# Kernel optimization log

Hardware: AMD Instinct MI355X
Metric: run time of the kernel (lower is better)

Reference implementation:

```python
import jax, jax.numpy as jnp
import numpy as np

# ---- config (matches init_kwargs) ----
L_LEVELS = 10          # int(log(8192/16)/log(2)) + 1
LEVEL_DIM = 4
BASE_RES = 16
LOG2_T = 21
BOUND = 2.0            # contract() output bound
DENSITY_BIAS = -1.0
RGB_PADDING = 0.001
DEG_VIEW = 4
PRIME1 = np.uint32(2654435761)
PRIME2 = np.uint32(805459861)


def _grid_meta():
    # torch-ngp GridEncoder layout: per-level scale = base*2^l - 1 (per_level_scale=2),
    # resolution = base*2^l, params = min(2^21, (res+1)^3) rounded up to multiple of 8.
    offsets, scales, res_list, sizes = [0], [], [], []
    for l in range(L_LEVELS):
        res = BASE_RES * (2 ** l)
        scales.append(float(res - 1))
        n = min(2 ** LOG2_T, (res + 1) ** 3)
        n = int(np.ceil(n / 8) * 8)
        res_list.append(res)
        sizes.append(n)
        offsets.append(offsets[-1] + n)
    return scales, res_list, sizes, offsets

GRID_SCALES, GRID_RES, GRID_SIZES, GRID_OFFSETS = _grid_meta()
TOTAL_PARAMS = GRID_OFFSETS[-1]  # 14995560
CORNERS = np.array([[(c >> d) & 1 for d in range(3)] for c in range(8)], dtype=np.int32)


def contract(x):
    # mipnerf360 contraction, output in [-2, 2]
    eps = jnp.finfo(x.dtype).eps
    x_mag_sq = jnp.maximum(eps, jnp.sum(x * x, axis=-1, keepdims=True))
    return jnp.where(x_mag_sq <= 1.0, x, ((2.0 * jnp.sqrt(x_mag_sq) - 1.0) / x_mag_sq) * x)


def pos_enc(x):
    # coord.pos_enc with identity, min_deg=0, max_deg=DEG_VIEW -> dim 3 + 3*2*4 = 27
    scales = 2.0 ** jnp.arange(DEG_VIEW, dtype=x.dtype)
    xb = (x[..., None, :] * scales[:, None]).reshape(x.shape[:-1] + (3 * DEG_VIEW,))
    four = jnp.sin(jnp.concatenate([xb, xb + 0.5 * jnp.pi], axis=-1))
    return jnp.concatenate([x, four], axis=-1)


def grid_encode(x01, embeddings):
    # x01: [N,3] in [0,1]; embeddings: [TOTAL_PARAMS, LEVEL_DIM]
    feats = []
    for l in range(L_LEVELS):
        pos = x01 * GRID_SCALES[l] + 0.5  # align_corners=False
        pos_floor = jnp.floor(pos)
        frac = pos - pos_floor            # trilinear weights, differentiable in x01
        pg = pos_floor.astype(jnp.int32)  # [N,3]
        res1 = GRID_RES[l] + 1
        size = GRID_SIZES[l]
        use_hash = (res1 ** 3) > size
        lvl_emb = embeddings[GRID_OFFSETS[l]:GRID_OFFSETS[l] + size]
        acc = jnp.zeros(x01.shape[:-1] + (LEVEL_DIM,), x01.dtype)
        for c in range(8):
            off = CORNERS[c]
            corner = pg + off[None, :]
            if use_hash:
                cu = corner.astype(jnp.uint32)
                idx = (cu[:, 0] ^ (cu[:, 1] * PRIME1) ^ (cu[:, 2] * PRIME2)) % jnp.uint32(size)
                idx = idx.astype(jnp.int32)
            else:
                idx = corner[:, 0] + corner[:, 1] * res1 + corner[:, 2] * (res1 * res1)
            w = jnp.prod(jnp.where(off[None, :] == 1, frac, 1.0 - frac), axis=-1)  # [N]
            acc = acc + w[:, None] * lvl_emb[idx]
        feats.append(acc)
    return jnp.concatenate(feats, axis=-1)  # [N, 40]


def setup_inputs() -> dict:
    key = jax.random.key(0)
    ks = jax.random.split(key, 10)
    R, S = 2048, 32
    coords = jax.random.normal(ks[0], (R, S, 3), jnp.float32) * 1.5
    viewdirs = jax.random.normal(ks[1], (R, 3), jnp.float32)
    viewdirs = viewdirs / jnp.linalg.norm(viewdirs, axis=-1, keepdims=True)
    embeddings = (jax.random.uniform(ks[2], (TOTAL_PARAMS, LEVEL_DIM), jnp.float32) * 2.0 - 1.0) * 1e-4

    def lin(k, fan_in, fan_out):
        k1, k2 = jax.random.split(k)
        lim = 1.0 / np.sqrt(fan_in)
        w = jax.random.uniform(k1, (fan_in, fan_out), jnp.float32, -lim, lim)
        b = jax.random.uniform(k2, (fan_out,), jnp.float32, -lim, lim)
        return w, b

    w_d1, b_d1 = lin(ks[3], L_LEVELS * LEVEL_DIM, 64)
    w_d2, b_d2 = lin(ks[4], 64, 256)
    DIR_DIM = 3 + 3 * 2 * DEG_VIEW  # 27
    w_r0, b_r0 = lin(ks[5], 256 + DIR_DIM, 256)          # 283 -> 256
    w_r1, b_r1 = lin(ks[6], 256 + 256 + DIR_DIM, 256)    # skip concat: 539 -> 256
    w_rgb, b_rgb = lin(ks[7], 256, 3)
    return dict(coords=coords, viewdirs=viewdirs, embeddings=embeddings,
                w_d1=w_d1, b_d1=b_d1, w_d2=w_d2, b_d2=b_d2,
                w_r0=w_r0, b_r0=b_r0, w_r1=w_r1, b_r1=b_r1,
                w_rgb=w_rgb, b_rgb=b_rgb)


def reference(coords, viewdirs, embeddings, w_d1, b_d1, w_d2, b_d2,
              w_r0, b_r0, w_r1, b_r1, w_rgb, b_rgb):
    shape = coords.shape[:-1]  # (rays, samples)
    cw = contract(coords) / BOUND          # coords_warped, in [-1, 1]
    x01 = (cw.reshape(-1, 3) + BOUND) / (2.0 * BOUND)  # encoder normalization with bound=2
    feats = grid_encode(x01, embeddings)               # [N, 40]
    h = jax.nn.relu(feats @ w_d1 + b_d1)
    x = h @ w_d2 + b_d2                                # [N, 256]
    raw_density = x[:, 0].reshape(shape)
    density = jax.nn.softplus(raw_density + DENSITY_BIAS)
    bottleneck = x.reshape(shape + (256,))
    dir_enc = pos_enc(viewdirs)                        # [rays, 27]
    dir_enc = jnp.broadcast_to(dir_enc[..., None, :], shape + (dir_enc.shape[-1],))
    inp = jnp.concatenate([bottleneck, dir_enc], axis=-1)  # [rays, S, 283]
    y = jax.nn.relu(inp @ w_r0 + b_r0)
    y = jnp.concatenate([y, inp], axis=-1)             # skip at layer i == skip_layer_dir == 0
    y = jax.nn.relu(y @ w_r1 + b_r1)
    rgb = jax.nn.sigmoid(y @ w_rgb + b_rgb)            # rgb_premultiplier=1, rgb_bias=0
    rgb = rgb * (1.0 + 2.0 * RGB_PADDING) - RGB_PADDING
    return cw, density, rgb
```

## Files before the change

kernel.cpp:

```cpp
#include <hip/hip_runtime.h>
#include <math.h>

#define NS 65536
#define NRAYS 2048

typedef __attribute__((ext_vector_type(8))) short short8;
typedef __attribute__((ext_vector_type(4))) float f32x4;
typedef unsigned short u16;

#define OFF_FEATS 0ull
#define OFF_HBF   10485760ull
#define OFF_DW0   85983232ull
#define OFF_DW1   88080384ull
#define OFF_WD2T  90177536ull
#define OFF_WR0T  90210304ull
#define OFF_WR1T  90341376ull

#define OUT_DENS 196608
#define OUT_RGB  262144

__device__ __forceinline__ u16 f2b(float f) {
    unsigned u = __builtin_bit_cast(unsigned, f);
    return (u16)((u + 0x7FFFu + ((u >> 16) & 1u)) >> 16);
}

__global__ __launch_bounds__(256) void cvt_weights(
    const float* __restrict__ w_d2, const float* __restrict__ w_r0,
    const float* __restrict__ w_r1, u16* __restrict__ wd2t,
    u16* __restrict__ wr0t, u16* __restrict__ wr1t)
{
    int idx = blockIdx.x * 256 + threadIdx.x;
    if (idx < 16384)  wd2t[idx] = f2b(w_d2[(idx & 63)  * 256 + (idx >> 6)]);
    if (idx < 65536)  wr0t[idx] = f2b(w_r0[(idx & 255) * 256 + (idx >> 8)]);
    if (idx < 131072) wr1t[idx] = f2b(w_r1[(idx & 511) * 256 + (idx >> 9)]);
}

__global__ __launch_bounds__(256) void dir_kernel(
    const float* __restrict__ viewdirs,
    const float* __restrict__ w_r0, const float* __restrict__ b_r0,
    const float* __restrict__ w_r1, const float* __restrict__ b_r1,
    float* __restrict__ dirW0, float* __restrict__ dirW1)
{
    __shared__ float de[27];
    int ray = blockIdx.x, t = threadIdx.x;
    if (t < 27) {
        float v;
        if (t < 3) v = viewdirs[3*ray + t];
        else {
            int k = (t - 3) % 12;
            float b = viewdirs[3*ray + (k % 3)] * (float)(1 << (k / 3));
            v = (t < 15) ? sinf(b) : sinf(b + 1.5707964f);
        }
        de[t] = v;
    }
    __syncthreads();
    float a0 = b_r0[t], a1 = b_r1[t];
#pragma unroll
    for (int d = 0; d < 27; ++d) {
        a0 = fmaf(de[d], w_r0[(256+d)*256 + t], a0);
        a1 = fmaf(de[d], w_r1[(512+d)*256 + t], a1);
    }
    dirW0[ray*256 + t] = a0;
    dirW1[ray*256 + t] = a1;
}

__global__ __launch_bounds__(256) void encode_kernel(
    const float* __restrict__ coords, const float* __restrict__ emb,
    float* __restrict__ cw_out, float* __restrict__ featsT)
{
    int t = threadIdx.x;
    int l = blockIdx.x >> 8;
    int i = ((blockIdx.x & 255) << 8) + t;
    float x = coords[3*i], y = coords[3*i+1], z = coords[3*i+2];
    float m2 = fmaxf(x*x + y*y + z*z, 1.1920928955078125e-07f);
    float cx = x, cy = y, cz = z;
    if (m2 > 1.0f) { float s = (2.0f*sqrtf(m2) - 1.0f)/m2; cx*=s; cy*=s; cz*=s; }
    cx *= 0.5f; cy *= 0.5f; cz *= 0.5f;
    if (l == 0) { cw_out[3*i]=cx; cw_out[3*i+1]=cy; cw_out[3*i+2]=cz; }
    float u0 = (cx + 2.0f)*0.25f, u1 = (cy + 2.0f)*0.25f, u2 = (cz + 2.0f)*0.25f;

    int res = 16 << l;
    int res1 = res + 1;
    float scale = (float)(res - 1);
    unsigned off = (l >= 3) ? 315496u + (unsigned)(l-3)*2097152u
                            : (l == 0 ? 0u : (l == 1 ? 4920u : 40864u));
    float p0 = u0*scale + 0.5f, p1 = u1*scale + 0.5f, p2 = u2*scale + 0.5f;
    float f0 = floorf(p0), f1 = floorf(p1), f2 = floorf(p2);
    float fr0 = p0-f0, fr1 = p1-f1, fr2 = p2-f2;
    unsigned g0 = (unsigned)(int)f0, g1 = (unsigned)(int)f1, g2 = (unsigned)(int)f2;
    float a0=0.f, a1=0.f, a2=0.f, a3=0.f;
    bool use_hash = (l >= 3);
#pragma unroll
    for (int c = 0; c < 8; ++c) {
        unsigned ox = c & 1u, oy = (c >> 1) & 1u, oz = (c >> 2) & 1u;
        unsigned qx = g0 + ox, qy = g1 + oy, qz = g2 + oz;
        unsigned idx;
        if (use_hash) idx = (qx ^ (qy*2654435761u) ^ (qz*805459861u)) & 2097151u;
        else          idx = qx + qy*(unsigned)res1 + qz*(unsigned)(res1*res1);
        const float4 e = *(const float4*)(emb + 4u*(off + idx));
        float w = (ox ? fr0 : 1.0f-fr0) * (oy ? fr1 : 1.0f-fr1) * (oz ? fr2 : 1.0f-fr2);
        a0 = fmaf(w, e.x, a0); a1 = fmaf(w, e.y, a1);
        a2 = fmaf(w, e.z, a2); a3 = fmaf(w, e.w, a3);
    }
    featsT[(4*l+0)*NS + i] = a0;
    featsT[(4*l+1)*NS + i] = a1;
    featsT[(4*l+2)*NS + i] = a2;
    featsT[(4*l+3)*NS + i] = a3;
}

__global__ __launch_bounds__(256) void gemm_d1_kernel(
    const float* __restrict__ featsT, const float* __restrict__ w_d1,
    const float* __restrict__ b_d1, const float* __restrict__ w_d2,
    const float* __restrict__ b_d2, u16* __restrict__ h_bf,
    float* __restrict__ dens)
{
    __shared__ float As[40][256];
    __shared__ float Ws[40*64];
    __shared__ float wc0[64];
    int t = threadIdx.x;
    int m0 = blockIdx.x * 256;
#pragma unroll
    for (int k = 0; k < 40; ++k) As[k][t] = featsT[k*NS + m0 + t];
#pragma unroll
    for (int i = 0; i < 10; ++i) Ws[i*256 + t] = w_d1[i*256 + t];
    if (t < 64) wc0[t] = w_d2[t*256];
    __syncthreads();
    int tn = t & 3, tm = t >> 2;
    float acc[4][16] = {};
#pragma unroll
    for (int k = 0; k < 40; ++k) {
        float4 a = *(const float4*)&As[k][tm*4];
        float av[4] = {a.x, a.y, a.z, a.w};
        const float4* wp = (const float4*)&Ws[k*64 + tn*16];
#pragma unroll
        for (int r = 0; r < 4; ++r) {
            float4 w = wp[r];
            float wv[4] = {w.x, w.y, w.z, w.w};
#pragma unroll
            for (int ii = 0; ii < 4; ++ii)
#pragma unroll
                for (int cc = 0; cc < 4; ++cc)
                    acc[ii][r*4+cc] = fmaf(av[ii], wv[cc], acc[ii][r*4+cc]);
        }
    }
    float p[4] = {0.f, 0.f, 0.f, 0.f};
#pragma unroll
    for (int jj = 0; jj < 16; ++jj) {
        int j = tn*16 + jj;
        float bj = b_d1[j], w0 = wc0[j];
#pragma unroll
        for (int ii = 0; ii < 4; ++ii) {
            float h = fmaxf(acc[ii][jj] + bj, 0.f);
            acc[ii][jj] = h;
            p[ii] = fmaf(h, w0, p[ii]);
        }
    }
#pragma unroll
    for (int ii = 0; ii < 4; ++ii) {
        int s = m0 + tm*4 + ii;
        unsigned u[8];
#pragma unroll
        for (int q = 0; q < 8; ++q)
            u[q] = (unsigned)f2b(acc[ii][2*q]) | ((unsigned)f2b(acc[ii][2*q+1]) << 16);
        uint4 v0 = {u[0], u[1], u[2], u[3]};
        uint4 v1 = {u[4], u[5], u[6], u[7]};
        *(uint4*)(h_bf + (size_t)s*64 + tn*16)     = v0;
        *(uint4*)(h_bf + (size_t)s*64 + tn*16 + 8) = v1;
    }
#pragma unroll
    for (int ii = 0; ii < 4; ++ii) {
        p[ii] += __shfl_xor(p[ii], 1, 64);
        p[ii] += __shfl_xor(p[ii], 2, 64);
    }
    if (tn == 0) {
        float b0 = b_d2[0];
#pragma unroll
        for (int ii = 0; ii < 4; ++ii) {
            float z = p[ii] + b0 - 1.0f;
            dens[m0 + tm*4 + ii] = fmaxf(z, 0.f) + log1pf(expf(-fabsf(z)));
        }
    }
}

#define MFMA __builtin_amdgcn_mfma_f32_16x16x32_bf16

__global__ __launch_bounds__(256, 2) void mfma_tail(
    const u16* __restrict__ h_bf, const u16* __restrict__ wd2t,
    const u16* __restrict__ w0t, const u16* __restrict__ w1t,
    const float* __restrict__ b_d2, const float* __restrict__ dirW0,
    const float* __restrict__ dirW1, const float* __restrict__ w_rgb,
    const float* __restrict__ b_rgb, float* __restrict__ rgb)
{
    __shared__ u16 tile[4][8192];
    int t = threadIdx.x, lane = t & 63, w = t >> 6;
    int m0 = blockIdx.x*128 + w*32;
    int rl = lane & 15, kg = (lane >> 4) * 8;
    int ro = (lane >> 4) * 4;
    f32x4 zero = {0.f,0.f,0.f,0.f};
    u16* tw = tile[w];
    const char* twc = (const char*)tw;
    unsigned swA = ((unsigned)(rl & 7)) << 4;

    f32x4 acc[2][16];

#pragma unroll
    for (int a = 0; a < 2; ++a)
#pragma unroll
        for (int b = 0; b < 16; ++b) acc[a][b] = zero;
    {
        const u16* pA0 = h_bf + (size_t)(m0 + rl)*64 + kg;
        const u16* pA1 = h_bf + (size_t)(m0 + 16 + rl)*64 + kg;
        const u16* pB  = wd2t + rl*64 + kg;
#pragma unroll
        for (int ks = 0; ks < 2; ++ks) {
            int kb = ks*32;
            short8 a0 = *(const short8*)(pA0 + kb);
            short8 a1 = *(const short8*)(pA1 + kb);
#pragma unroll
            for (int nt = 0; nt < 16; ++nt) {
                short8 b = *(const short8*)(pB + nt*1024 + kb);
                acc[0][nt] = MFMA(a0, b, acc[0][nt], 0, 0, 0);
                acc[1][nt] = MFMA(a1, b, acc[1][nt], 0, 0, 0);
            }
        }
    }
#pragma unroll
    for (int nt = 0; nt < 16; ++nt) {
        int col = nt*16 + rl;
        float bias = b_d2[col];
#pragma unroll
        for (int mt = 0; mt < 2; ++mt)
#pragma unroll
            for (int r = 0; r < 4; ++r) {
                int row = mt*16 + ro + r;
                unsigned byte = (unsigned)(row*512 + col*2) ^ ((unsigned)(row & 7) << 4);
                tw[byte >> 1] = f2b(acc[mt][nt][r] + bias);
            }
    }
    __syncthreads();
    short8 xa0[8], xa1[8];
#pragma unroll
    for (int ks = 0; ks < 8; ++ks) {
        unsigned base = (unsigned)((ks*32 + kg)*2);
        xa0[ks] = *(const short8*)(twc + (((unsigned)(rl*512)      + base) ^ swA));
        xa1[ks] = *(const short8*)(twc + (((unsigned)((16+rl)*512) + base) ^ swA));
    }
    __syncthreads();

#pragma unroll
    for (int a = 0; a < 2; ++a)
#pragma unroll
        for (int b = 0; b < 16; ++b) acc[a][b] = zero;
    {
        const u16* pB = w0t + rl*256 + kg;
#pragma unroll
        for (int ks = 0; ks < 8; ++ks) {
            int kb = ks*32;
#pragma unroll
            for (int nt = 0; nt < 16; ++nt) {
                short8 b = *(const short8*)(pB + nt*4096 + kb);
                acc[0][nt] = MFMA(xa0[ks], b, acc[0][nt], 0, 0, 0);
                acc[1][nt] = MFMA(xa1[ks], b, acc[1][nt], 0, 0, 0);
            }
        }
    }
    {
        const float* dir0 = dirW0 + (m0 >> 5)*256;
#pragma unroll
        for (int nt = 0; nt < 16; ++nt) {
            int col = nt*16 + rl;
            float bias = dir0[col];
#pragma unroll
            for (int mt = 0; mt < 2; ++mt)
#pragma unroll
                for (int r = 0; r < 4; ++r) {
                    int row = mt*16 + ro + r;
                    unsigned byte = (unsigned)(row*512 + col*2) ^ ((unsigned)(row & 7) << 4);
                    tw[byte >> 1] = f2b(fmaxf(acc[mt][nt][r] + bias, 0.f));
                }
        }
    }
    __syncthreads();

#pragma unroll
    for (int a = 0; a < 2; ++a)
#pragma unroll
        for (int b = 0; b < 16; ++b) acc[a][b] = zero;
    {
        const u16* pB = w1t + rl*512 + kg;
#pragma unroll
        for (int ks = 0; ks < 8; ++ks) {
            int kb = 256 + ks*32;
#pragma unroll
            for (int nt = 0; nt < 16; ++nt) {
                short8 b = *(const short8*)(pB + nt*8192 + kb);
                acc[0][nt] = MFMA(xa0[ks], b, acc[0][nt], 0, 0, 0);
                acc[1][nt] = MFMA(xa1[ks], b, acc[1][nt], 0, 0, 0);
            }
        }
#pragma unroll
        for (int ks = 0; ks < 8; ++ks) {
            int kb = ks*32;
            unsigned base = (unsigned)((kb + kg)*2);
            short8 ya0 = *(const short8*)(twc + (((unsigned)(rl*512)      + base) ^ swA));
            short8 ya1 = *(const short8*)(twc + (((unsigned)((16+rl)*512) + base) ^ swA));
#pragma unroll
            for (int nt = 0; nt < 16; ++nt) {
                short8 b = *(const short8*)(pB + nt*8192 + kb);
                acc[0][nt] = MFMA(ya0, b, acc[0][nt], 0, 0, 0);
                acc[1][nt] = MFMA(ya1, b, acc[1][nt], 0, 0, 0);
            }
        }
    }

    const float* dir1 = dirW1 + (m0 >> 5)*256;
    float p[2][4][3];
#pragma unroll
    for (int mt = 0; mt < 2; ++mt)
#pragma unroll
        for (int r = 0; r < 4; ++r)
            p[mt][r][0] = p[mt][r][1] = p[mt][r][2] = 0.f;
#pragma unroll
    for (int nt = 0; nt < 16; ++nt) {
        int col = nt*16 + rl;
        float dv = dir1[col];
        float w0 = w_rgb[col*3], w1 = w_rgb[col*3+1], w2 = w_rgb[col*3+2];
#pragma unroll
        for (int mt = 0; mt < 2; ++mt)
#pragma unroll
            for (int r = 0; r < 4; ++r) {
                float y1 = fmaxf(acc[mt][nt][r] + dv, 0.f);
                p[mt][r][0] = fmaf(y1, w0, p[mt][r][0]);
                p[mt][r][1] = fmaf(y1, w1, p[mt][r][1]);
                p[mt][r][2] = fmaf(y1, w2, p[mt][r][2]);
            }
    }
#pragma unroll
    for (int mask = 1; mask < 16; mask <<= 1)
#pragma unroll
        for (int mt = 0; mt < 2; ++mt)
#pragma unroll
            for (int r = 0; r < 4; ++r)
#pragma unroll
                for (int c = 0; c < 3; ++c)
                    p[mt][r][c] += __shfl_xor(p[mt][r][c], mask, 64);
    if (rl == 0) {
#pragma unroll
        for (int mt = 0; mt < 2; ++mt)
#pragma unroll
            for (int r = 0; r < 4; ++r) {
                int row = m0 + mt*16 + ro + r;
#pragma unroll
                for (int c = 0; c < 3; ++c) {
                    float v = p[mt][r][c] + b_rgb[c];
                    float sg = 1.0f / (1.0f + expf(-v));
                    rgb[row*3 + c] = sg * 1.002f - 0.001f;
                }
            }
    }
}

extern "C" void kernel_launch(void* const* d_in, const int* in_sizes, int n_in,
                              void* d_out, int out_size, void* d_ws, size_t ws_size,
                              hipStream_t stream)
{
    const float* coords   = (const float*)d_in[0];
    const float* viewdirs = (const float*)d_in[1];
    const float* emb      = (const float*)d_in[2];
    const float* w_d1     = (const float*)d_in[3];
    const float* b_d1     = (const float*)d_in[4];
    const float* w_d2     = (const float*)d_in[5];
    const float* b_d2     = (const float*)d_in[6];
    const float* w_r0     = (const float*)d_in[7];
    const float* b_r0     = (const float*)d_in[8];
    const float* w_r1     = (const float*)d_in[9];
    const float* b_r1     = (const float*)d_in[10];
    const float* w_rgb    = (const float*)d_in[11];
    const float* b_rgb    = (const float*)d_in[12];

    float* out  = (float*)d_out;
    float* cw   = out;
    float* dens = out + OUT_DENS;
    float* rgb  = out + OUT_RGB;

    char* wsB = (char*)d_ws;
    float* featsT = (float*)(wsB + OFF_FEATS);
    u16*   h_bf   = (u16*)(wsB + OFF_HBF);
    float* dirW0  = (float*)(wsB + OFF_DW0);
    float* dirW1  = (float*)(wsB + OFF_DW1);
    u16*   wd2t   = (u16*)(wsB + OFF_WD2T);
    u16*   wr0t   = (u16*)(wsB + OFF_WR0T);
    u16*   wr1t   = (u16*)(wsB + OFF_WR1T);

    cvt_weights<<<512, 256, 0, stream>>>(w_d2, w_r0, w_r1, wd2t, wr0t, wr1t);
    dir_kernel<<<NRAYS, 256, 0, stream>>>(viewdirs, w_r0, b_r0, w_r1, b_r1, dirW0, dirW1);
    encode_kernel<<<2560, 256, 0, stream>>>(coords, emb, cw, featsT);
    gemm_d1_kernel<<<NS/256, 256, 0, stream>>>(featsT, w_d1, b_d1, w_d2, b_d2, h_bf, dens);
    mfma_tail<<<NS/128, 256, 0, stream>>>(h_bf, wd2t, wr0t, wr1t, b_d2,
                                          dirW0, dirW1, w_rgb, b_rgb, rgb);
}
```

Measured before the change: 511.6 us.

## Split MFMA tail N-dimension across waves sharing one 32-row tile

Each block now handles 32 rows instead of 128, and its four waves split the 256 output columns (64 each) rather than each wave owning 32 rows and all columns. Activations are shared through two LDS tiles (X and Y), and the per-wave partial RGB dot products are reduced through a small shared array. This cuts accumulator registers from 32 to 8 f32x4 per lane, raising occupancy and making 4x more blocks. In exchange every block rereads the full weight matrices, so weight traffic per row rises, and extra block-wide syncs are added.

```diff
diff --git a/kernel.cpp b/kernel.cpp
--- a/kernel.cpp
+++ b/kernel.cpp
@@ -184,49 +184,51 @@
 
 #define MFMA __builtin_amdgcn_mfma_f32_16x16x32_bf16
 
-__global__ __launch_bounds__(256, 2) void mfma_tail(
+__global__ __launch_bounds__(256) void mfma_tail(
     const u16* __restrict__ h_bf, const u16* __restrict__ wd2t,
     const u16* __restrict__ w0t, const u16* __restrict__ w1t,
     const float* __restrict__ b_d2, const float* __restrict__ dirW0,
     const float* __restrict__ dirW1, const float* __restrict__ w_rgb,
     const float* __restrict__ b_rgb, float* __restrict__ rgb)
 {
-    __shared__ u16 tile[4][8192];
+    __shared__ u16 tileX[8192];
+    __shared__ u16 tileY[8192];
+    __shared__ float pp[4][32][3];
     int t = threadIdx.x, lane = t & 63, w = t >> 6;
-    int m0 = blockIdx.x*128 + w*32;
+    int m0 = blockIdx.x * 32;
     int rl = lane & 15, kg = (lane >> 4) * 8;
     int ro = (lane >> 4) * 4;
+    unsigned swA = ((unsigned)(rl & 7)) << 4;
+    const char* txc = (const char*)tileX;
+    const char* tyc = (const char*)tileY;
     f32x4 zero = {0.f,0.f,0.f,0.f};
-    u16* tw = tile[w];
-    const char* twc = (const char*)tw;
-    unsigned swA = ((unsigned)(rl & 7)) << 4;
-
-    f32x4 acc[2][16];
+
+    f32x4 acc[2][4];
 
 #pragma unroll
     for (int a = 0; a < 2; ++a)
 #pragma unroll
-        for (int b = 0; b < 16; ++b) acc[a][b] = zero;
+        for (int b = 0; b < 4; ++b) acc[a][b] = zero;
     {
         const u16* pA0 = h_bf + (size_t)(m0 + rl)*64 + kg;
         const u16* pA1 = h_bf + (size_t)(m0 + 16 + rl)*64 + kg;
-        const u16* pB  = wd2t + rl*64 + kg;
+        const u16* pBd = wd2t + (w*64 + rl)*64 + kg;
 #pragma unroll
         for (int ks = 0; ks < 2; ++ks) {
             int kb = ks*32;
             short8 a0 = *(const short8*)(pA0 + kb);
             short8 a1 = *(const short8*)(pA1 + kb);
 #pragma unroll
-            for (int nt = 0; nt < 16; ++nt) {
-                short8 b = *(const short8*)(pB + nt*1024 + kb);
+            for (int nt = 0; nt < 4; ++nt) {
+                short8 b = *(const short8*)(pBd + nt*1024 + kb);
                 acc[0][nt] = MFMA(a0, b, acc[0][nt], 0, 0, 0);
                 acc[1][nt] = MFMA(a1, b, acc[1][nt], 0, 0, 0);
             }
         }
     }
 #pragma unroll
-    for (int nt = 0; nt < 16; ++nt) {
-        int col = nt*16 + rl;
+    for (int nt = 0; nt < 4; ++nt) {
+        int col = w*64 + nt*16 + rl;
         float bias = b_d2[col];
 #pragma unroll
         for (int mt = 0; mt < 2; ++mt)
@@ -234,41 +236,36 @@
             for (int r = 0; r < 4; ++r) {
                 int row = mt*16 + ro + r;
                 unsigned byte = (unsigned)(row*512 + col*2) ^ ((unsigned)(row & 7) << 4);
-                tw[byte >> 1] = f2b(acc[mt][nt][r] + bias);
+                tileX[byte >> 1] = f2b(acc[mt][nt][r] + bias);
             }
     }
     __syncthreads();
-    short8 xa0[8], xa1[8];
-#pragma unroll
-    for (int ks = 0; ks < 8; ++ks) {
-        unsigned base = (unsigned)((ks*32 + kg)*2);
-        xa0[ks] = *(const short8*)(twc + (((unsigned)(rl*512)      + base) ^ swA));
-        xa1[ks] = *(const short8*)(twc + (((unsigned)((16+rl)*512) + base) ^ swA));
-    }
-    __syncthreads();
 
 #pragma unroll
     for (int a = 0; a < 2; ++a)
 #pragma unroll
-        for (int b = 0; b < 16; ++b) acc[a][b] = zero;
+        for (int b = 0; b < 4; ++b) acc[a][b] = zero;
     {
-        const u16* pB = w0t + rl*256 + kg;
+        const u16* pB0 = w0t + (w*64 + rl)*256 + kg;
 #pragma unroll
         for (int ks = 0; ks < 8; ++ks) {
             int kb = ks*32;
-#pragma unroll
-            for (int nt = 0; nt < 16; ++nt) {
-                short8 b = *(const short8*)(pB + nt*4096 + kb);
-                acc[0][nt] = MFMA(xa0[ks], b, acc[0][nt], 0, 0, 0);
-                acc[1][nt] = MFMA(xa1[ks], b, acc[1][nt], 0, 0, 0);
+            unsigned base = (unsigned)((kb + kg)*2);
+            short8 a0 = *(const short8*)(txc + (((unsigned)(rl*512)      + base) ^ swA));
+            short8 a1 = *(const short8*)(txc + (((unsigned)((16+rl)*512) + base) ^ swA));
+#pragma unroll
+            for (int nt = 0; nt < 4; ++nt) {
+                short8 b = *(const short8*)(pB0 + nt*4096 + kb);
+                acc[0][nt] = MFMA(a0, b, acc[0][nt], 0, 0, 0);
+                acc[1][nt] = MFMA(a1, b, acc[1][nt], 0, 0, 0);
             }
         }
     }
     {
         const float* dir0 = dirW0 + (m0 >> 5)*256;
 #pragma unroll
-        for (int nt = 0; nt < 16; ++nt) {
-            int col = nt*16 + rl;
+        for (int nt = 0; nt < 4; ++nt) {
+            int col = w*64 + nt*16 + rl;
             float bias = dir0[col];
 #pragma unroll
             for (int mt = 0; mt < 2; ++mt)
@@ -276,7 +273,7 @@
                 for (int r = 0; r < 4; ++r) {
                     int row = mt*16 + ro + r;
                     unsigned byte = (unsigned)(row*512 + col*2) ^ ((unsigned)(row & 7) << 4);
-                    tw[byte >> 1] = f2b(fmaxf(acc[mt][nt][r] + bias, 0.f));
+                    tileY[byte >> 1] = f2b(fmaxf(acc[mt][nt][r] + bias, 0.f));
                 }
         }
     }
@@ -285,78 +282,88 @@
 #pragma unroll
     for (int a = 0; a < 2; ++a)
 #pragma unroll
-        for (int b = 0; b < 16; ++b) acc[a][b] = zero;
+        for (int b = 0; b < 4; ++b) acc[a][b] = zero;
     {
-        const u16* pB = w1t + rl*512 + kg;
+        const u16* pB1 = w1t + (w*64 + rl)*512 + kg;
 #pragma unroll
         for (int ks = 0; ks < 8; ++ks) {
             int kb = 256 + ks*32;
-#pragma unroll
-            for (int nt = 0; nt < 16; ++nt) {
-                short8 b = *(const short8*)(pB + nt*8192 + kb);
-                acc[0][nt] = MFMA(xa0[ks], b, acc[0][nt], 0, 0, 0);
-                acc[1][nt] = MFMA(xa1[ks], b, acc[1][nt], 0, 0, 0);
+            unsigned base = (unsigned)((ks*32 + kg)*2);
+            short8 a0 = *(const short8*)(txc + (((unsigned)(rl*512)      + base) ^ swA));
+            short8 a1 = *(const short8*)(txc + (((unsigned)((16+rl)*512) + base) ^ swA));
+#pragma unroll
+            for (int nt = 0; nt < 4; ++nt) {
+                short8 b = *(const short8*)(pB1 + nt*8192 + kb);
+                acc[0][nt] = MFMA(a0, b, acc[0][nt], 0, 0, 0);
+                acc[1][nt] = MFMA(a1, b, acc[1][nt], 0, 0, 0);
             }
         }
 #pragma unroll
         for (int ks = 0; ks < 8; ++ks) {
             int kb = ks*32;
             unsigned base = (unsigned)((kb + kg)*2);
-            short8 ya0 = *(const short8*)(twc + (((unsigned)(rl*512)      + base) ^ swA));
-            short8 ya1 = *(const short8*)(twc + (((unsigned)((16+rl)*512) + base) ^ swA));
-#pragma unroll
-            for (int nt = 0; nt < 16; ++nt) {
-                short8 b = *(const short8*)(pB + nt*8192 + kb);
-                acc[0][nt] = MFMA(ya0, b, acc[0][nt], 0, 0, 0);
-                acc[1][nt] = MFMA(ya1, b, acc[1][nt], 0, 0, 0);
+            short8 a0 = *(const short8*)(tyc + (((unsigned)(rl*512)      + base) ^ swA));
+            short8 a1 = *(const short8*)(tyc + (((unsigned)((16+rl)*512) + base) ^ swA));
+#pragma unroll
+            for (int nt = 0; nt < 4; ++nt) {
+                short8 b = *(const short8*)(pB1 + nt*8192 + kb);
+                acc[0][nt] = MFMA(a0, b, acc[0][nt], 0, 0, 0);
+                acc[1][nt] = MFMA(a1, b, acc[1][nt], 0, 0, 0);
             }
         }
     }
 
-    const float* dir1 = dirW1 + (m0 >> 5)*256;
-    float p[2][4][3];
-#pragma unroll
-    for (int mt = 0; mt < 2; ++mt)
-#pragma unroll
-        for (int r = 0; r < 4; ++r)
-            p[mt][r][0] = p[mt][r][1] = p[mt][r][2] = 0.f;
-#pragma unroll
-    for (int nt = 0; nt < 16; ++nt) {
-        int col = nt*16 + rl;
-        float dv = dir1[col];
-        float w0 = w_rgb[col*3], w1 = w_rgb[col*3+1], w2 = w_rgb[col*3+2];
+    {
+        const float* dir1 = dirW1 + (m0 >> 5)*256;
+        float p[2][4][3];
 #pragma unroll
         for (int mt = 0; mt < 2; ++mt)
 #pragma unroll
-            for (int r = 0; r < 4; ++r) {
-                float y1 = fmaxf(acc[mt][nt][r] + dv, 0.f);
-                p[mt][r][0] = fmaf(y1, w0, p[mt][r][0]);
-                p[mt][r][1] = fmaf(y1, w1, p[mt][r][1]);
-                p[mt][r][2] = fmaf(y1, w2, p[mt][r][2]);
-            }
-    }
-#pragma unroll
-    for (int mask = 1; mask < 16; mask <<= 1)
-#pragma unroll
-        for (int mt = 0; mt < 2; ++mt)
-#pragma unroll
             for (int r = 0; r < 4; ++r)
-#pragma unroll
-                for (int c = 0; c < 3; ++c)
-                    p[mt][r][c] += __shfl_xor(p[mt][r][c], mask, 64);
-    if (rl == 0) {
-#pragma unroll
-        for (int mt = 0; mt < 2; ++mt)
-#pragma unroll
-            for (int r = 0; r < 4; ++r) {
-                int row = m0 + mt*16 + ro + r;
-#pragma unroll
-                for (int c = 0; c < 3; ++c) {
-                    float v = p[mt][r][c] + b_rgb[c];
-                    float sg = 1.0f / (1.0f + expf(-v));
-                    rgb[row*3 + c] = sg * 1.002f - 0.001f;
+                p[mt][r][0] = p[mt][r][1] = p[mt][r][2] = 0.f;
+#pragma unroll
+        for (int nt = 0; nt < 4; ++nt) {
+            int col = w*64 + nt*16 + rl;
+            float dv = dir1[col];
+            float w0 = w_rgb[col*3], w1 = w_rgb[col*3+1], w2 = w_rgb[col*3+2];
+#pragma unroll
+            for (int mt = 0; mt < 2; ++mt)
+#pragma unroll
+                for (int r = 0; r < 4; ++r) {
+                    float y1 = fmaxf(acc[mt][nt][r] + dv, 0.f);
+                    p[mt][r][0] = fmaf(y1, w0, p[mt][r][0]);
+                    p[mt][r][1] = fmaf(y1, w1, p[mt][r][1]);
+                    p[mt][r][2] = fmaf(y1, w2, p[mt][r][2]);
                 }
-            }
+        }
+#pragma unroll
+        for (int mask = 1; mask < 16; mask <<= 1)
+#pragma unroll
+            for (int mt = 0; mt < 2; ++mt)
+#pragma unroll
+                for (int r = 0; r < 4; ++r)
+#pragma unroll
+                    for (int c = 0; c < 3; ++c)
+                        p[mt][r][c] += __shfl_xor(p[mt][r][c], mask, 64);
+        if (rl == 0) {
+#pragma unroll
+            for (int mt = 0; mt < 2; ++mt)
+#pragma unroll
+                for (int r = 0; r < 4; ++r) {
+                    int row = mt*16 + ro + r;
+                    pp[w][row][0] = p[mt][r][0];
+                    pp[w][row][1] = p[mt][r][1];
+                    pp[w][row][2] = p[mt][r][2];
+                }
+        }
+    }
+    __syncthreads();
+    if (t < 96) {
+        int row = t / 3, c = t - row*3;
+        float v = pp[0][row][c] + pp[1][row][c] + pp[2][row][c] + pp[3][row][c]
+                + b_rgb[c];
+        float sg = 1.0f / (1.0f + expf(-v));
+        rgb[(m0 + row)*3 + c] = sg * 1.002f - 0.001f;
     }
 }
 
@@ -396,6 +403,6 @@
     dir_kernel<<<NRAYS, 256, 0, stream>>>(viewdirs, w_r0, b_r0, w_r1, b_r1, dirW0, dirW1);
     encode_kernel<<<2560, 256, 0, stream>>>(coords, emb, cw, featsT);
     gemm_d1_kernel<<<NS/256, 256, 0, stream>>>(featsT, w_d1, b_d1, w_d2, b_d2, h_bf, dens);
-    mfma_tail<<<NS/128, 256, 0, stream>>>(h_bf, wd2t, wr0t, wr1t, b_d2,
-                                          dirW0, dirW1, w_rgb, b_rgb, rgb);
-}
+    mfma_tail<<<NS/32, 256, 0, stream>>>(h_bf, wd2t, wr0t, wr1t, b_d2,
+                                         dirW0, dirW1, w_rgb, b_rgb, rgb);
+}
```

After: 462.2 us. -9.7%, faster.
